# Optimization experiments

Measured on AMD Instinct MI355X. Metric: run time of the kernel, lower is better.

The kernel has to match this reference:

```python
import jax, jax.numpy as jnp
import numpy as np

NEG_SLOPE = 0.01  # torch nn.LeakyReLU default


def setup_inputs() -> dict:
    key = jax.random.key(0)
    k1, k2 = jax.random.split(key)
    B, L, N = 32, 512, 1024
    X = jax.random.normal(k1, (B, L, N), dtype=jnp.float32)
    W = jax.random.normal(k2, (1, 2 * L), dtype=jnp.float32) * (1.0 / np.sqrt(2 * L))
    return {"X": X, "W": W}


def reference(X, W):
    # X: [B, L, N]; W: [1, 2L] weight of Linear(2L, 1, bias=False)
    L = X.shape[1]
    N = X.shape[2]
    w1 = W[0, :L]   # applied to X[:, :, i]
    w2 = W[0, L:]   # applied to X[:, :, j]
    s1 = jnp.einsum('bln,l->bn', X, w1)  # [B, N]
    s2 = jnp.einsum('bln,l->bn', X, w2)  # [B, N]
    # e[b,i,j] = leaky_relu(s1[b,i] + s2[b,j]) for i != j, 0 on the diagonal
    e = jax.nn.leaky_relu(s1[:, :, None] + s2[:, None, :], NEG_SLOPE)  # [B, N, N]
    diag = jnp.eye(N, dtype=bool)
    e = jnp.where(diag[None, :, :], 0.0, e)
    # softmax over dim=1 (over i), matching torch.softmax(e, dim=1)
    alpha = jax.nn.softmax(e, axis=1)  # [B, N, N]
    # h = bmm(alpha, X^T)^T: h[b,l,i] = sum_j alpha[b,i,j] * X[b,l,j]
    h = jnp.einsum('bij,blj->bli', alpha, X)  # [B, L, N]
    return jax.nn.sigmoid(h)
```

## Files before the change

### kernel.cpp

```cpp
#include <hip/hip_runtime.h>
#include <hip/hip_bf16.h>

#define BATCH 32
#define LSEQ  512
#define NDIM  1024
#define NSPLIT 16

typedef __attribute__((ext_vector_type(8))) short bf16x8;
typedef __attribute__((ext_vector_type(4))) float f32x4;

__device__ __forceinline__ unsigned short f2bf(float x) {
    __hip_bfloat16 h = __float2bfloat16(x);
    return __builtin_bit_cast(unsigned short, h);
}

__global__ __launch_bounds__(256) void prep_kernel(
    const float* __restrict__ X, const float* __restrict__ W,
    unsigned short* __restrict__ Xb, float* __restrict__ P1, float* __restrict__ P2)
{
    __shared__ float sw[2 * LSEQ];
    int tid = threadIdx.x;
    for (int i = tid; i < 2 * LSEQ; i += 256) sw[i] = W[i];
    __syncthreads();

    int b  = blockIdx.y;
    int sp = blockIdx.x;
    int l0 = sp * (LSEQ / NSPLIT);
    size_t base = ((size_t)b * LSEQ + l0) * NDIM + tid * 4;
    const float* xp = X + base;
    unsigned short* xbp = Xb + base;

    float a0=0,a1=0,a2=0,a3=0, c0=0,c1=0,c2=0,c3=0;
    for (int l = 0; l < LSEQ / NSPLIT; ++l) {
        float4 x = *(const float4*)(xp + (size_t)l * NDIM);
        float w1 = sw[l0 + l], w2 = sw[LSEQ + l0 + l];
        a0 = fmaf(x.x, w1, a0); a1 = fmaf(x.y, w1, a1);
        a2 = fmaf(x.z, w1, a2); a3 = fmaf(x.w, w1, a3);
        c0 = fmaf(x.x, w2, c0); c1 = fmaf(x.y, w2, c1);
        c2 = fmaf(x.z, w2, c2); c3 = fmaf(x.w, w2, c3);
        ushort4 u; u.x = f2bf(x.x); u.y = f2bf(x.y); u.z = f2bf(x.z); u.w = f2bf(x.w);
        *(ushort4*)(xbp + (size_t)l * NDIM) = u;
    }
    size_t po = ((size_t)sp * BATCH + b) * NDIM + tid * 4;
    *(float4*)(P1 + po) = make_float4(a0, a1, a2, a3);
    *(float4*)(P2 + po) = make_float4(c0, c1, c2, c3);
}

__global__ __launch_bounds__(256) void stats_kernel(
    const float* __restrict__ P1, const float* __restrict__ P2,
    float* __restrict__ s1, float* __restrict__ s2, float* __restrict__ rd)
{
    __shared__ float s1s[NDIM];
    __shared__ float s2s[128];
    int t = threadIdx.x;
    int b = blockIdx.x >> 3, sl = blockIdx.x & 7;
    int j0 = sl * 128;

    #pragma unroll
    for (int q = 0; q < 4; ++q) {
        int n = q * 256 + t;
        float a = 0.f;
        #pragma unroll
        for (int sp = 0; sp < NSPLIT; ++sp)
            a += P1[((size_t)sp * BATCH + b) * NDIM + n];
        s1s[n] = a;
        if (sl == 0) s1[b * NDIM + n] = a;
    }
    if (t < 128) {
        int j = j0 + t;
        float c = 0.f;
        #pragma unroll
        for (int sp = 0; sp < NSPLIT; ++sp)
            c += P2[((size_t)sp * BATCH + b) * NDIM + j];
        s2s[t] = c;
        s2[b * NDIM + j] = c;
    }
    __syncthreads();

    int jl = t >> 1, half = t & 1;
    int jg = j0 + jl;
    float s2j = s2s[jl];
    float sum = 0.f;
    int i0 = half * 512;
    for (int i = i0; i < i0 + 512; ++i) {
        float v = s1s[i] + s2j;
        v = fmaxf(v, 0.01f * v);
        if (i == jg) v = 0.f;
        sum += __expf(v);
    }
    sum += __shfl_xor(sum, 1);
    if (half == 0) rd[b * NDIM + jg] = 1.0f / sum;
}

__global__ __launch_bounds__(256) void btgen_kernel(
    const float* __restrict__ s1, const float* __restrict__ s2,
    const float* __restrict__ rd, unsigned short* __restrict__ Bt)
{
    int wid = threadIdx.x >> 6, lane = threadIdx.x & 63;
    int r = blockIdx.x * 4 + wid;
    int b = r >> 10, i = r & 1023;
    float s1i = s1[r];
    const float* s2b = s2 + b * NDIM;
    const float* rdb = rd + b * NDIM;
    unsigned short* outp = Bt + (size_t)r * NDIM;

    #pragma unroll
    for (int q = 0; q < 2; ++q) {
        int j0 = q * 512 + lane * 8;
        float sv[8], rv[8];
        #pragma unroll
        for (int h = 0; h < 2; ++h) {
            float4 s4 = *(const float4*)(s2b + j0 + h * 4);
            float4 r4 = *(const float4*)(rdb + j0 + h * 4);
            sv[h*4+0]=s4.x; sv[h*4+1]=s4.y; sv[h*4+2]=s4.z; sv[h*4+3]=s4.w;
            rv[h*4+0]=r4.x; rv[h*4+1]=r4.y; rv[h*4+2]=r4.z; rv[h*4+3]=r4.w;
        }
        bf16x8 v;
        #pragma unroll
        for (int k = 0; k < 8; ++k) {
            float e = s1i + sv[k];
            e = fmaxf(e, 0.01f * e);
            if (j0 + k == i) e = 0.f;
            v[k] = (short)f2bf(__expf(e) * rv[k]);
        }
        *(bf16x8*)&outp[j0] = v;
    }
}

#define WAITVM(n) asm volatile("s_waitcnt vmcnt(" #n ")" ::: "memory")
#define FENCE()   asm volatile("" ::: "memory")

#define DO_STAGE(bufi) {                                                        \
    _Pragma("unroll")                                                           \
    for (int j = 0; j < 4; ++j) {                                               \
        __builtin_amdgcn_global_load_lds(                                       \
            (const __attribute__((address_space(1))) void*)srcp[j],             \
            (__attribute__((address_space(3))) void*)(LdsC + (bufi) * 32768 +   \
                                                      ldst0 + j * 8192),        \
            16, 0, 0);                                                          \
        srcp[j] += 64;                       \
    } }

#define COMPUTE(bufi) {                                                         \
    const char* Lb = LdsC + (bufi) * 32768;                                     \
    bf16x8 av[8]; bf16x8 bv[4];                                                 \
    _Pragma("unroll")                                                           \
    for (int mi = 0; mi < 8; ++mi)                                              \
        av[mi] = *(const bf16x8*)(Lb + abase0 + mi * 2048);                     \
    _Pragma("unroll")                                                           \
    for (int ni = 0; ni < 4; ++ni)                                              \
        bv[ni] = *(const bf16x8*)(Lb + bbase0 + ni * 2048);                     \
    __builtin_amdgcn_s_setprio(1);                                              \
    _Pragma("unroll")                                                           \
    for (int ni = 0; ni < 4; ++ni)                                              \
        _Pragma("unroll")                                                       \
        for (int mi = 0; mi < 8; ++mi)                                          \
            acc[mi][ni] = __builtin_amdgcn_mfma_f32_16x16x32_bf16(              \
                av[mi], bv[ni], acc[mi][ni], 0, 0, 0);                          \
    __builtin_amdgcn_s_setprio(0);                                              \
}

__global__ __launch_bounds__(512, 2) void gemm_kernel(
    const unsigned short* __restrict__ Xb, const unsigned short* __restrict__ Bt,
    float* __restrict__ out)
{
    __shared__ __align__(16) unsigned short LDSU[65536];
    char* LdsC = (char*)LDSU;

    const int tid = threadIdx.x, lane = tid & 63, wid = tid >> 6;
    const int wm = wid >> 2, wn = wid & 3;

    int flat  = blockIdx.x;
    int xcd   = flat & 7;
    int p     = flat >> 3;
    int b     = (p >> 3) * 8 + xcd;
    int inner = p & 7;
    int mt = inner & 1, nt = inner >> 1;
    int l0 = mt * 256, n0 = nt * 256;

    const char* XgB = (const char*)(Xb + ((size_t)b * LSEQ + l0) * NDIM);
    const char* BgB = (const char*)(Bt + ((size_t)b * NDIM + n0) * NDIM);

    const char* srcp[4];
    #pragma unroll
    for (int j = 0; j < 4; ++j) {
        int c = tid + j * 512;
        int r = c >> 3, slot = c & 7;
        int off = (slot * 16) ^ ((r & 7) << 4);
        srcp[j] = (off < 64) ? XgB + (size_t)r * 2048 + off
                             : BgB + (size_t)r * 2048 + (off - 64);
    }
    const int ldst0 = wid * 1024;

    const int rsel = lane & 15, kq = lane >> 4;
    const int swz  = (rsel & 7) << 4;
    const int abase0 = wm * 16384 + rsel * 128 + ((kq * 16) ^ swz);
    const int bbase0 = wn * 8192  + rsel * 128 + (((64 + kq * 16)) ^ swz);

    f32x4 acc[8][4] = {};

    DO_STAGE(0); DO_STAGE(1); DO_STAGE(2);

    for (int t = 0; t < 29; ++t) {
        WAITVM(8);
        __builtin_amdgcn_s_barrier();
        FENCE();
        DO_STAGE((t + 3) & 3);
        COMPUTE(t & 3);
    }
    WAITVM(8); __builtin_amdgcn_s_barrier(); FENCE(); COMPUTE(1);
    WAITVM(4); __builtin_amdgcn_s_barrier(); FENCE(); COMPUTE(2);
    WAITVM(0); __builtin_amdgcn_s_barrier(); FENCE(); COMPUTE(3);

    float* outb = out + ((size_t)b * LSEQ + l0) * NDIM + n0;
    const int rq = lane >> 4, cl = lane & 15;
    #pragma unroll
    for (int mi = 0; mi < 8; ++mi)
        #pragma unroll
        for (int ni = 0; ni < 4; ++ni) {
            int col = wn * 64 + ni * 16 + cl;
            #pragma unroll
            for (int r2 = 0; r2 < 4; ++r2) {
                int row = wm * 128 + mi * 16 + rq * 4 + r2;
                float v = acc[mi][ni][r2];
                outb[(size_t)row * NDIM + col] = 1.0f / (1.0f + __expf(-v));
            }
        }
}

#undef WAITVM
#undef FENCE
#undef DO_STAGE
#undef COMPUTE

extern "C" void kernel_launch(void* const* d_in, const int* in_sizes, int n_in,
                              void* d_out, int out_size, void* d_ws, size_t ws_size,
                              hipStream_t stream) {
    (void)in_sizes; (void)n_in; (void)out_size; (void)ws_size;
    const float* X = (const float*)d_in[0];
    const float* W = (const float*)d_in[1];
    float* out = (float*)d_out;

    float* s1 = (float*)d_ws;
    float* s2 = s1 + BATCH * NDIM;
    float* rd = s2 + BATCH * NDIM;
    float* P1 = rd + BATCH * NDIM;
    float* P2 = P1 + (size_t)NSPLIT * BATCH * NDIM;
    unsigned short* Xb = (unsigned short*)(P2 + (size_t)NSPLIT * BATCH * NDIM);
    unsigned short* Bt = Xb + (size_t)BATCH * LSEQ * NDIM;

    prep_kernel<<<dim3(NSPLIT, BATCH), 256, 0, stream>>>(X, W, Xb, P1, P2);
    stats_kernel<<<256, 256, 0, stream>>>(P1, P2, s1, s2, rd);
    btgen_kernel<<<(BATCH * NDIM) / 4, 256, 0, stream>>>(s1, s2, rd, Bt);
    gemm_kernel<<<256, 512, 0, stream>>>(Xb, Bt, out);
}
```

Before: 183.7 us.

## Split GEMM K-tile compute into two half phases with interleaved prefetch

Each K-step of the GEMM loop now runs as two halves of 4 M-subtiles each. Each half loads its A fragments, issues two of the four async global-to-LDS prefetch loads, and waits on LDS counters behind a sched barrier. A workgroup barrier sits between the halves. The aim is to spread the global load issue across the MFMA work and to lower the number of live A registers, in return for an extra barrier per iteration and explicit waitcnt/scheduling constraints.

```diff
diff --git a/kernel.cpp b/kernel.cpp
--- a/kernel.cpp
+++ b/kernel.cpp
@@ -128,35 +128,51 @@
 }
 
 #define WAITVM(n) asm volatile("s_waitcnt vmcnt(" #n ")" ::: "memory")
+#define LGKM0()   do { asm volatile("s_waitcnt lgkmcnt(0)" ::: "memory"); \
+                       __builtin_amdgcn_sched_barrier(0); } while (0)
 #define FENCE()   asm volatile("" ::: "memory")
 
-#define DO_STAGE(bufi) {                                                        \
-    _Pragma("unroll")                                                           \
-    for (int j = 0; j < 4; ++j) {                                               \
-        __builtin_amdgcn_global_load_lds(                                       \
-            (const __attribute__((address_space(1))) void*)srcp[j],             \
-            (__attribute__((address_space(3))) void*)(LdsC + (bufi) * 32768 +   \
-                                                      ldst0 + j * 8192),        \
-            16, 0, 0);                                                          \
-        srcp[j] += 64;                       \
-    } }
-
-#define COMPUTE(bufi) {                                                         \
+#define STAGE1(bufi, j_) {                                                      \
+    __builtin_amdgcn_global_load_lds(                                           \
+        (const __attribute__((address_space(1))) void*)srcp[j_],                \
+        (__attribute__((address_space(3))) void*)(LdsC + (bufi) * 32768 +       \
+                                                  ldst0 + (j_) * 8192),         \
+        16, 0, 0);                                                              \
+    srcp[j_] += 64;                                   \
+}
+
+#define TILE(bufi, pfbuf, PF) {                                                 \
     const char* Lb = LdsC + (bufi) * 32768;                                     \
-    bf16x8 av[8]; bf16x8 bv[4];                                                 \
-    _Pragma("unroll")                                                           \
-    for (int mi = 0; mi < 8; ++mi)                                              \
-        av[mi] = *(const bf16x8*)(Lb + abase0 + mi * 2048);                     \
+    bf16x8 av[4], bv[4];                                                        \
     _Pragma("unroll")                                                           \
     for (int ni = 0; ni < 4; ++ni)                                              \
         bv[ni] = *(const bf16x8*)(Lb + bbase0 + ni * 2048);                     \
+    _Pragma("unroll")                                                           \
+    for (int mi = 0; mi < 4; ++mi)                                              \
+        av[mi] = *(const bf16x8*)(Lb + abase0 + mi * 2048);                     \
+    if (PF) { STAGE1(pfbuf, 0); STAGE1(pfbuf, 1); }                             \
+    LGKM0();                                                                    \
     __builtin_amdgcn_s_setprio(1);                                              \
     _Pragma("unroll")                                                           \
     for (int ni = 0; ni < 4; ++ni)                                              \
         _Pragma("unroll")                                                       \
-        for (int mi = 0; mi < 8; ++mi)                                          \
+        for (int mi = 0; mi < 4; ++mi)                                          \
             acc[mi][ni] = __builtin_amdgcn_mfma_f32_16x16x32_bf16(              \
                 av[mi], bv[ni], acc[mi][ni], 0, 0, 0);                          \
+    __builtin_amdgcn_s_setprio(0);                                              \
+    FENCE(); __builtin_amdgcn_s_barrier(); FENCE();                             \
+    _Pragma("unroll")                                                           \
+    for (int mi = 0; mi < 4; ++mi)                                              \
+        av[mi] = *(const bf16x8*)(Lb + abase0 + (4 + mi) * 2048);               \
+    if (PF) { STAGE1(pfbuf, 2); STAGE1(pfbuf, 3); }                             \
+    LGKM0();                                                                    \
+    __builtin_amdgcn_s_setprio(1);                                              \
+    _Pragma("unroll")                                                           \
+    for (int ni = 0; ni < 4; ++ni)                                              \
+        _Pragma("unroll")                                                       \
+        for (int mi = 0; mi < 4; ++mi)                                          \
+            acc[4 + mi][ni] = __builtin_amdgcn_mfma_f32_16x16x32_bf16(          \
+                av[mi], bv[ni], acc[4 + mi][ni], 0, 0, 0);                      \
     __builtin_amdgcn_s_setprio(0);                                              \
 }
 
@@ -199,18 +215,18 @@
 
     f32x4 acc[8][4] = {};
 
-    DO_STAGE(0); DO_STAGE(1); DO_STAGE(2);
+    { STAGE1(0,0); STAGE1(0,1); STAGE1(0,2); STAGE1(0,3); }
+    { STAGE1(1,0); STAGE1(1,1); STAGE1(1,2); STAGE1(1,3); }
+    { STAGE1(2,0); STAGE1(2,1); STAGE1(2,2); STAGE1(2,3); }
 
     for (int t = 0; t < 29; ++t) {
         WAITVM(8);
-        __builtin_amdgcn_s_barrier();
-        FENCE();
-        DO_STAGE((t + 3) & 3);
-        COMPUTE(t & 3);
-    }
-    WAITVM(8); __builtin_amdgcn_s_barrier(); FENCE(); COMPUTE(1);
-    WAITVM(4); __builtin_amdgcn_s_barrier(); FENCE(); COMPUTE(2);
-    WAITVM(0); __builtin_amdgcn_s_barrier(); FENCE(); COMPUTE(3);
+        FENCE(); __builtin_amdgcn_s_barrier(); FENCE();
+        TILE(t & 3, (t + 3) & 3, 1);
+    }
+    WAITVM(8); FENCE(); __builtin_amdgcn_s_barrier(); FENCE(); TILE(1, 0, 0);
+    WAITVM(4); FENCE(); __builtin_amdgcn_s_barrier(); FENCE(); TILE(2, 0, 0);
+    WAITVM(0); FENCE(); __builtin_amdgcn_s_barrier(); FENCE(); TILE(3, 0, 0);
 
     float* outb = out + ((size_t)b * LSEQ + l0) * NDIM + n0;
     const int rq = lane >> 4, cl = lane & 15;
@@ -229,9 +245,10 @@
 }
 
 #undef WAITVM
+#undef LGKM0
 #undef FENCE
-#undef DO_STAGE
-#undef COMPUTE
+#undef STAGE1
+#undef TILE
 
 extern "C" void kernel_launch(void* const* d_in, const int* in_sizes, int n_in,
                               void* d_out, int out_size, void* d_ws, size_t ws_size,
```

New measurement: 185.9 us. About the same (+1.2%).

## Restructure GEMM to K=128 double-buffered tiles with interleaved staging; widen prep grid

Applied to the files above, without the earlier changes.

The GEMM main loop moves from a 4-stage ring of K=32 stages to two 64KB buffers holding K=128 tiles, each split into two K-halves. Global-to-LDS loads for upcoming tiles are interleaved between MFMA groups, with barriers and an lgkmcnt wait around each group, and the LDS swizzle is redone for 64-byte rows. Separately, prep_kernel gets a z dimension of 2 so each thread handles 2 columns instead of 4, doubling the block count to raise parallelism. The extra barriers per tile add synchronisation cost and the hand-written staging order must be correct to avoid races.

```diff
diff --git a/kernel.cpp b/kernel.cpp
--- a/kernel.cpp
+++ b/kernel.cpp
@@ -25,25 +25,26 @@
 
     int b  = blockIdx.y;
     int sp = blockIdx.x;
+    int z  = blockIdx.z;
     int l0 = sp * (LSEQ / NSPLIT);
-    size_t base = ((size_t)b * LSEQ + l0) * NDIM + tid * 4;
+    int n  = z * 512 + tid * 2;
+    size_t base = ((size_t)b * LSEQ + l0) * NDIM + n;
     const float* xp = X + base;
     unsigned short* xbp = Xb + base;
 
-    float a0=0,a1=0,a2=0,a3=0, c0=0,c1=0,c2=0,c3=0;
+    float a0 = 0, a1 = 0, c0 = 0, c1 = 0;
+    #pragma unroll 4
     for (int l = 0; l < LSEQ / NSPLIT; ++l) {
-        float4 x = *(const float4*)(xp + (size_t)l * NDIM);
+        float2 x = *(const float2*)(xp + (size_t)l * NDIM);
         float w1 = sw[l0 + l], w2 = sw[LSEQ + l0 + l];
         a0 = fmaf(x.x, w1, a0); a1 = fmaf(x.y, w1, a1);
-        a2 = fmaf(x.z, w1, a2); a3 = fmaf(x.w, w1, a3);
         c0 = fmaf(x.x, w2, c0); c1 = fmaf(x.y, w2, c1);
-        c2 = fmaf(x.z, w2, c2); c3 = fmaf(x.w, w2, c3);
-        ushort4 u; u.x = f2bf(x.x); u.y = f2bf(x.y); u.z = f2bf(x.z); u.w = f2bf(x.w);
-        *(ushort4*)(xbp + (size_t)l * NDIM) = u;
-    }
-    size_t po = ((size_t)sp * BATCH + b) * NDIM + tid * 4;
-    *(float4*)(P1 + po) = make_float4(a0, a1, a2, a3);
-    *(float4*)(P2 + po) = make_float4(c0, c1, c2, c3);
+        ushort2 u; u.x = f2bf(x.x); u.y = f2bf(x.y);
+        *(ushort2*)(xbp + (size_t)l * NDIM) = u;
+    }
+    size_t po = ((size_t)sp * BATCH + b) * NDIM + n;
+    *(float2*)(P1 + po) = make_float2(a0, a1);
+    *(float2*)(P2 + po) = make_float2(c0, c1);
 }
 
 __global__ __launch_bounds__(256) void stats_kernel(
@@ -128,36 +129,56 @@
 }
 
 #define WAITVM(n) asm volatile("s_waitcnt vmcnt(" #n ")" ::: "memory")
-#define FENCE()   asm volatile("" ::: "memory")
-
-#define DO_STAGE(bufi) {                                                        \
-    _Pragma("unroll")                                                           \
-    for (int j = 0; j < 4; ++j) {                                               \
-        __builtin_amdgcn_global_load_lds(                                       \
-            (const __attribute__((address_space(1))) void*)srcp[j],             \
-            (__attribute__((address_space(3))) void*)(LdsC + (bufi) * 32768 +   \
-                                                      ldst0 + j * 8192),        \
-            16, 0, 0);                                                          \
-        srcp[j] += 64;                       \
-    } }
-
-#define COMPUTE(bufi) {                                                         \
-    const char* Lb = LdsC + (bufi) * 32768;                                     \
-    bf16x8 av[8]; bf16x8 bv[4];                                                 \
-    _Pragma("unroll")                                                           \
-    for (int mi = 0; mi < 8; ++mi)                                              \
-        av[mi] = *(const bf16x8*)(Lb + abase0 + mi * 2048);                     \
-    _Pragma("unroll")                                                           \
-    for (int ni = 0; ni < 4; ++ni)                                              \
-        bv[ni] = *(const bf16x8*)(Lb + bbase0 + ni * 2048);                     \
-    __builtin_amdgcn_s_setprio(1);                                              \
-    _Pragma("unroll")                                                           \
-    for (int ni = 0; ni < 4; ++ni)                                              \
-        _Pragma("unroll")                                                       \
-        for (int mi = 0; mi < 8; ++mi)                                          \
-            acc[mi][ni] = __builtin_amdgcn_mfma_f32_16x16x32_bf16(              \
-                av[mi], bv[ni], acc[mi][ni], 0, 0, 0);                          \
-    __builtin_amdgcn_s_setprio(0);                                              \
+#define LGKM0()   asm volatile("s_waitcnt lgkmcnt(0)" ::: "memory")
+#define BARF()    do { asm volatile("" ::: "memory");                          \
+                       __builtin_amdgcn_s_barrier();                           \
+                       asm volatile("" ::: "memory"); } while (0)
+
+#define STAGE(PTR, OPB, KH, TT, DB) do {                                       \
+    const char* s_ = (PTR) + (TT) * 128 + (KH) * 64;                           \
+    __builtin_amdgcn_global_load_lds(                                          \
+        (const __attribute__((address_space(1))) void*)s_,                     \
+        (__attribute__((address_space(3))) void*)(LdsC + (DB) * 65536 + (OPB)  \
+            + (KH) * 16384 + tid * 16), 16, 0, 0);                             \
+    __builtin_amdgcn_global_load_lds(                                          \
+        (const __attribute__((address_space(1))) void*)(s_ + 262144),          \
+        (__attribute__((address_space(3))) void*)(LdsC + (DB) * 65536 + (OPB)  \
+            + (KH) * 16384 + 8192 + tid * 16), 16, 0, 0);                      \
+} while (0)
+
+#define RDA(DB, KH, MI) (*(const bf16x8*)(LdsC + (DB) * 65536 +                \
+                          (KH) * 16384 + abase + (MI) * 1024))
+#define RDB(DB, KH, NI) (*(const bf16x8*)(LdsC + (DB) * 65536 + 32768 +        \
+                          (KH) * 16384 + bbase + (NI) * 1024))
+
+#define MFMA16(NH)                                                             \
+    __builtin_amdgcn_s_setprio(1);                                             \
+    _Pragma("unroll")                                                          \
+    for (int ni2 = 0; ni2 < 2; ++ni2)                                          \
+        _Pragma("unroll")                                                      \
+        for (int mi = 0; mi < 8; ++mi)                                         \
+            acc[mi][(NH) * 2 + ni2] = __builtin_amdgcn_mfma_f32_16x16x32_bf16( \
+                av[mi], bv[ni2], acc[mi][(NH) * 2 + ni2], 0, 0, 0);            \
+    __builtin_amdgcn_s_setprio(0);
+
+#define TILE(TT, DB, SM) {                                                     \
+    bf16x8 av[8], bv[2];                                                       \
+    _Pragma("unroll")                                                          \
+    for (int mi = 0; mi < 8; ++mi) av[mi] = RDA(DB, 0, mi);                    \
+    bv[0] = RDB(DB, 0, 0); bv[1] = RDB(DB, 0, 1);                              \
+    if ((SM) >= 1) STAGE(pB, 32768, 1, (TT) + 1, (DB) ^ 1);                    \
+    BARF(); LGKM0(); MFMA16(0); BARF();                                        \
+    bv[0] = RDB(DB, 0, 2); bv[1] = RDB(DB, 0, 3);                              \
+    if ((SM) >= 2) STAGE(pA, 0, 0, (TT) + 2, DB);                              \
+    BARF(); LGKM0(); MFMA16(1); BARF();                                        \
+    _Pragma("unroll")                                                          \
+    for (int mi = 0; mi < 8; ++mi) av[mi] = RDA(DB, 1, mi);                    \
+    bv[0] = RDB(DB, 1, 0); bv[1] = RDB(DB, 1, 1);                              \
+    if ((SM) >= 2) STAGE(pB, 32768, 0, (TT) + 2, DB);                          \
+    BARF(); LGKM0(); MFMA16(0); BARF();                                        \
+    bv[0] = RDB(DB, 1, 2); bv[1] = RDB(DB, 1, 3);                              \
+    if ((SM) >= 2) STAGE(pA, 0, 1, (TT) + 2, DB);                              \
+    BARF(); LGKM0(); MFMA16(1);                                                \
 }
 
 __global__ __launch_bounds__(512, 2) void gemm_kernel(
@@ -167,7 +188,8 @@
     __shared__ __align__(16) unsigned short LDSU[65536];
     char* LdsC = (char*)LDSU;
 
-    const int tid = threadIdx.x, lane = tid & 63, wid = tid >> 6;
+    const int tid = threadIdx.x, lane = tid & 63;
+    const int wid = tid >> 6;
     const int wm = wid >> 2, wn = wid & 3;
 
     int flat  = blockIdx.x;
@@ -181,36 +203,36 @@
     const char* XgB = (const char*)(Xb + ((size_t)b * LSEQ + l0) * NDIM);
     const char* BgB = (const char*)(Bt + ((size_t)b * NDIM + n0) * NDIM);
 
-    const char* srcp[4];
-    #pragma unroll
-    for (int j = 0; j < 4; ++j) {
-        int c = tid + j * 512;
-        int r = c >> 3, slot = c & 7;
-        int off = (slot * 16) ^ ((r & 7) << 4);
-        srcp[j] = (off < 64) ? XgB + (size_t)r * 2048 + off
-                             : BgB + (size_t)r * 2048 + (off - 64);
-    }
-    const int ldst0 = wid * 1024;
+    {
+    }
+    const int srow  = tid >> 2;
+    const int sswz  = ((srow >> 1) & 3) << 4;
+    const int sloff = ((tid & 3) * 16) ^ sswz;
+    const char* pA = XgB + (size_t)srow * 2048 + sloff;
+    const char* pB = BgB + (size_t)srow * 2048 + sloff;
 
     const int rsel = lane & 15, kq = lane >> 4;
-    const int swz  = (rsel & 7) << 4;
-    const int abase0 = wm * 16384 + rsel * 128 + ((kq * 16) ^ swz);
-    const int bbase0 = wn * 8192  + rsel * 128 + (((64 + kq * 16)) ^ swz);
+    const int swz2 = ((rsel >> 1) & 3) << 4;
+    const int abase = (wm * 128 + rsel) * 64 + ((kq * 16) ^ swz2);
+    const int bbase = (wn * 64  + rsel) * 64 + ((kq * 16) ^ swz2);
 
     f32x4 acc[8][4] = {};
 
-    DO_STAGE(0); DO_STAGE(1); DO_STAGE(2);
-
-    for (int t = 0; t < 29; ++t) {
-        WAITVM(8);
-        __builtin_amdgcn_s_barrier();
-        FENCE();
-        DO_STAGE((t + 3) & 3);
-        COMPUTE(t & 3);
-    }
-    WAITVM(8); __builtin_amdgcn_s_barrier(); FENCE(); COMPUTE(1);
-    WAITVM(4); __builtin_amdgcn_s_barrier(); FENCE(); COMPUTE(2);
-    WAITVM(0); __builtin_amdgcn_s_barrier(); FENCE(); COMPUTE(3);
+    STAGE(pA, 0,     0, 0, 0);
+    STAGE(pB, 32768, 0, 0, 0);
+    STAGE(pA, 0,     1, 0, 0);
+    STAGE(pB, 32768, 1, 0, 0);
+    STAGE(pA, 0,     0, 1, 1);
+    STAGE(pB, 32768, 0, 1, 1);
+    STAGE(pA, 0,     1, 1, 1);
+
+    for (int pp = 0; pp < 7; ++pp) {
+        int t0 = 2 * pp;
+        WAITVM(6); BARF(); TILE(t0,     0, 2);
+        WAITVM(6); BARF(); TILE(t0 + 1, 1, 2);
+    }
+    WAITVM(6); BARF(); TILE(14, 0, 1);
+    WAITVM(0); BARF(); TILE(15, 1, 0);
 
     float* outb = out + ((size_t)b * LSEQ + l0) * NDIM + n0;
     const int rq = lane >> 4, cl = lane & 15;
@@ -229,9 +251,13 @@
 }
 
 #undef WAITVM
-#undef FENCE
-#undef DO_STAGE
-#undef COMPUTE
+#undef LGKM0
+#undef BARF
+#undef STAGE
+#undef RDA
+#undef RDB
+#undef MFMA16
+#undef TILE
 
 extern "C" void kernel_launch(void* const* d_in, const int* in_sizes, int n_in,
                               void* d_out, int out_size, void* d_ws, size_t ws_size,
@@ -249,7 +275,7 @@
     unsigned short* Xb = (unsigned short*)(P2 + (size_t)NSPLIT * BATCH * NDIM);
     unsigned short* Bt = Xb + (size_t)BATCH * LSEQ * NDIM;
 
-    prep_kernel<<<dim3(NSPLIT, BATCH), 256, 0, stream>>>(X, W, Xb, P1, P2);
+    prep_kernel<<<dim3(NSPLIT, BATCH, 2), 256, 0, stream>>>(X, W, Xb, P1, P2);
     stats_kernel<<<256, 256, 0, stream>>>(P1, P2, s1, s2, rd);
     btgen_kernel<<<(BATCH * NDIM) / 4, 256, 0, stream>>>(s1, s2, rd, Bt);
     gemm_kernel<<<256, 512, 0, stream>>>(Xb, Bt, out);
```

Result: no change. 186.2 us (+1.4%).

## Fuse attention-weight generation into GEMM, computing B tiles in LDS on the fly

Applied to the files above, without the earlier changes.

Drops the separate btgen kernel and the bf16 Bt matrix in global memory. The GEMM now builds each softmax-weight tile in LDS from s1, s2 and log-reciprocal denominators, while only X tiles are streamed from global memory. The normalisation is folded into the exponent as exp(v - log sum). The pipeline becomes double-buffered with 128-byte k-steps and interleaves B generation between the MFMA halves. Prep now uses NSPLIT 32 with an unrolled loop. This removes roughly a 64MB write and read of Bt, but adds exp work inside the GEMM, full waits each iteration, and much larger LDS use (136KB), which may limit occupancy below the declared 2 blocks.

```diff
diff --git a/kernel.cpp b/kernel.cpp
--- a/kernel.cpp
+++ b/kernel.cpp
@@ -4,7 +4,7 @@
 #define BATCH 32
 #define LSEQ  512
 #define NDIM  1024
-#define NSPLIT 16
+#define NSPLIT 32
 
 typedef __attribute__((ext_vector_type(8))) short bf16x8;
 typedef __attribute__((ext_vector_type(4))) float f32x4;
@@ -31,6 +31,7 @@
     unsigned short* xbp = Xb + base;
 
     float a0=0,a1=0,a2=0,a3=0, c0=0,c1=0,c2=0,c3=0;
+    #pragma unroll
     for (int l = 0; l < LSEQ / NSPLIT; ++l) {
         float4 x = *(const float4*)(xp + (size_t)l * NDIM);
         float w1 = sw[l0 + l], w2 = sw[LSEQ + l0 + l];
@@ -48,7 +49,7 @@
 
 __global__ __launch_bounds__(256) void stats_kernel(
     const float* __restrict__ P1, const float* __restrict__ P2,
-    float* __restrict__ s1, float* __restrict__ s2, float* __restrict__ rd)
+    float* __restrict__ s1, float* __restrict__ s2, float* __restrict__ lrd)
 {
     __shared__ float s1s[NDIM];
     __shared__ float s2s[128];
@@ -89,83 +90,79 @@
         sum += __expf(v);
     }
     sum += __shfl_xor(sum, 1);
-    if (half == 0) rd[b * NDIM + jg] = 1.0f / sum;
-}
-
-__global__ __launch_bounds__(256) void btgen_kernel(
-    const float* __restrict__ s1, const float* __restrict__ s2,
-    const float* __restrict__ rd, unsigned short* __restrict__ Bt)
-{
-    int wid = threadIdx.x >> 6, lane = threadIdx.x & 63;
-    int r = blockIdx.x * 4 + wid;
-    int b = r >> 10, i = r & 1023;
-    float s1i = s1[r];
-    const float* s2b = s2 + b * NDIM;
-    const float* rdb = rd + b * NDIM;
-    unsigned short* outp = Bt + (size_t)r * NDIM;
-
-    #pragma unroll
-    for (int q = 0; q < 2; ++q) {
-        int j0 = q * 512 + lane * 8;
-        float sv[8], rv[8];
-        #pragma unroll
-        for (int h = 0; h < 2; ++h) {
-            float4 s4 = *(const float4*)(s2b + j0 + h * 4);
-            float4 r4 = *(const float4*)(rdb + j0 + h * 4);
-            sv[h*4+0]=s4.x; sv[h*4+1]=s4.y; sv[h*4+2]=s4.z; sv[h*4+3]=s4.w;
-            rv[h*4+0]=r4.x; rv[h*4+1]=r4.y; rv[h*4+2]=r4.z; rv[h*4+3]=r4.w;
-        }
-        bf16x8 v;
-        #pragma unroll
-        for (int k = 0; k < 8; ++k) {
-            float e = s1i + sv[k];
-            e = fmaxf(e, 0.01f * e);
-            if (j0 + k == i) e = 0.f;
-            v[k] = (short)f2bf(__expf(e) * rv[k]);
-        }
-        *(bf16x8*)&outp[j0] = v;
-    }
-}
-
-#define WAITVM(n) asm volatile("s_waitcnt vmcnt(" #n ")" ::: "memory")
-#define FENCE()   asm volatile("" ::: "memory")
-
-#define DO_STAGE(bufi) {                                                        \
-    _Pragma("unroll")                                                           \
-    for (int j = 0; j < 4; ++j) {                                               \
-        __builtin_amdgcn_global_load_lds(                                       \
-            (const __attribute__((address_space(1))) void*)srcp[j],             \
-            (__attribute__((address_space(3))) void*)(LdsC + (bufi) * 32768 +   \
-                                                      ldst0 + j * 8192),        \
-            16, 0, 0);                                                          \
-        srcp[j] += 64;                       \
+    if (half == 0) lrd[b * NDIM + jg] = -__logf(sum);
+}
+
+#define WAITVM0() asm volatile("s_waitcnt vmcnt(0)" ::: "memory")
+#define LGKM0()   asm volatile("s_waitcnt lgkmcnt(0)" ::: "memory")
+#define BARF()    do { asm volatile("" ::: "memory");                          \
+                       __builtin_amdgcn_s_barrier();                           \
+                       asm volatile("" ::: "memory"); } while (0)
+
+#define STAGE(DB) {                                                            \
+    _Pragma("unroll")                                                          \
+    for (int j = 0; j < 4; ++j) {                                              \
+        __builtin_amdgcn_global_load_lds(                                      \
+            (const __attribute__((address_space(1))) void*)srcp[j],            \
+            (__attribute__((address_space(3))) void*)(LdsC + (DB) * 32768 +    \
+                tid * 16 + j * 8192), 16, 0, 0);                               \
+        srcp[j] += 128;                                  \
     } }
 
-#define COMPUTE(bufi) {                                                         \
-    const char* Lb = LdsC + (bufi) * 32768;                                     \
-    bf16x8 av[8]; bf16x8 bv[4];                                                 \
-    _Pragma("unroll")                                                           \
-    for (int mi = 0; mi < 8; ++mi)                                              \
-        av[mi] = *(const bf16x8*)(Lb + abase0 + mi * 2048);                     \
-    _Pragma("unroll")                                                           \
-    for (int ni = 0; ni < 4; ++ni)                                              \
-        bv[ni] = *(const bf16x8*)(Lb + bbase0 + ni * 2048);                     \
-    __builtin_amdgcn_s_setprio(1);                                              \
-    _Pragma("unroll")                                                           \
-    for (int ni = 0; ni < 4; ++ni)                                              \
-        _Pragma("unroll")                                                       \
-        for (int mi = 0; mi < 8; ++mi)                                          \
-            acc[mi][ni] = __builtin_amdgcn_mfma_f32_16x16x32_bf16(              \
-                av[mi], bv[ni], acc[mi][ni], 0, 0, 0);                          \
-    __builtin_amdgcn_s_setprio(0);                                              \
+#define BGEN(T2, DB) {                                                         \
+    const float* s2p = s2s + (T2) * 64 + jb * 8;                               \
+    const float* ldp = lrds + (T2) * 64 + jb * 8;                              \
+    float4 sa = *(const float4*)(s2p);                                         \
+    float4 sb = *(const float4*)(s2p + 4);                                     \
+    float4 la = *(const float4*)(ldp);                                         \
+    float4 lb = *(const float4*)(ldp + 4);                                     \
+    float sv[8] = {sa.x,sa.y,sa.z,sa.w,sb.x,sb.y,sb.z,sb.w};                   \
+    float lv[8] = {la.x,la.y,la.z,la.w,lb.x,lb.y,lb.z,lb.w};                   \
+    int jg0 = (T2) * 64 + jb * 8;                                              \
+    _Pragma("unroll")                                                          \
+    for (int q = 0; q < 4; ++q) {                                              \
+        int rloc = wid * 32 + q * 8 + il;                                      \
+        int ig = n0 + rloc;                                                    \
+        bf16x8 w;                                                              \
+        _Pragma("unroll")                                                      \
+        for (int h = 0; h < 8; ++h) {                                          \
+            float v = s1q[q] + sv[h];                                          \
+            v = fmaxf(v, 0.01f * v);                           \
+            if (jg0 + h == ig) v = 0.f;                  \
+            w[h] = (short)f2bf(__expf(v + lv[h]));                             \
+        }                                                                      \
+        *(bf16x8*)(LdsC + 65536 + (DB) * 32768 + rloc * 128 +                  \
+                   ((jb * 16) ^ (il << 4))) = w;                               \
+    } }
+
+#define COMPUTE_KS(DB, KOF) {                                                  \
+    bf16x8 av[8], bv[4];                                                       \
+    _Pragma("unroll")                                                          \
+    for (int mi = 0; mi < 8; ++mi)                                             \
+        av[mi] = *(const bf16x8*)(LdsC + (DB) * 32768 + arow + mi * 2048 +     \
+                                  (KOF));                                      \
+    _Pragma("unroll")                                                          \
+    for (int ni = 0; ni < 4; ++ni)                                             \
+        bv[ni] = *(const bf16x8*)(LdsC + 65536 + (DB) * 32768 + brow +         \
+                                  ni * 2048 + (KOF));                          \
+    __builtin_amdgcn_s_setprio(1);                                             \
+    _Pragma("unroll")                                                          \
+    for (int ni = 0; ni < 4; ++ni)                                             \
+        _Pragma("unroll")                                                      \
+        for (int mi = 0; mi < 8; ++mi)                                         \
+            acc[mi][ni] = __builtin_amdgcn_mfma_f32_16x16x32_bf16(             \
+                av[mi], bv[ni], acc[mi][ni], 0, 0, 0);                         \
+    __builtin_amdgcn_s_setprio(0);                                             \
 }
 
 __global__ __launch_bounds__(512, 2) void gemm_kernel(
-    const unsigned short* __restrict__ Xb, const unsigned short* __restrict__ Bt,
+    const unsigned short* __restrict__ Xb, const float* __restrict__ s1,
+    const float* __restrict__ s2, const float* __restrict__ lrd,
     float* __restrict__ out)
 {
-    __shared__ __align__(16) unsigned short LDSU[65536];
-    char* LdsC = (char*)LDSU;
+    __shared__ __align__(16) char LdsC[139264];
+    float* s2s  = (float*)(LdsC + 131072);
+    float* lrds = (float*)(LdsC + 135168);
 
     const int tid = threadIdx.x, lane = tid & 63, wid = tid >> 6;
     const int wm = wid >> 2, wn = wid & 3;
@@ -179,38 +176,53 @@
     int l0 = mt * 256, n0 = nt * 256;
 
     const char* XgB = (const char*)(Xb + ((size_t)b * LSEQ + l0) * NDIM);
-    const char* BgB = (const char*)(Bt + ((size_t)b * NDIM + n0) * NDIM);
 
     const char* srcp[4];
     #pragma unroll
     for (int j = 0; j < 4; ++j) {
         int c = tid + j * 512;
         int r = c >> 3, slot = c & 7;
-        int off = (slot * 16) ^ ((r & 7) << 4);
-        srcp[j] = (off < 64) ? XgB + (size_t)r * 2048 + off
-                             : BgB + (size_t)r * 2048 + (off - 64);
-    }
-    const int ldst0 = wid * 1024;
+        srcp[j] = XgB + (size_t)r * 2048 + ((slot * 16) ^ ((r & 7) << 4));
+    }
 
     const int rsel = lane & 15, kq = lane >> 4;
     const int swz  = (rsel & 7) << 4;
-    const int abase0 = wm * 16384 + rsel * 128 + ((kq * 16) ^ swz);
-    const int bbase0 = wn * 8192  + rsel * 128 + (((64 + kq * 16)) ^ swz);
+    const int kof0 = (kq * 16) ^ swz;
+    const int kof1 = (64 + kq * 16) ^ swz;
+    const int arow = (wm * 128 + rsel) * 128;
+    const int brow = (wn * 64 + rsel) * 128;
+
+    const int jb = lane & 7, il = lane >> 3;
+
+    {
+        const float* s2g = s2 + (size_t)b * NDIM;
+        const float* ldg = lrd + (size_t)b * NDIM;
+        if (tid < 256) *(float4*)(s2s + tid * 4) = *(const float4*)(s2g + tid * 4);
+        else *(float4*)(lrds + (tid - 256) * 4) = *(const float4*)(ldg + (tid - 256) * 4);
+    }
+    STAGE(0);
+    __syncthreads();
+
+    float s1q[4];
+    #pragma unroll
+    for (int q = 0; q < 4; ++q)
+        s1q[q] = s1[(size_t)b * NDIM + n0 + wid * 32 + q * 8 + il];
 
     f32x4 acc[8][4] = {};
 
-    DO_STAGE(0); DO_STAGE(1); DO_STAGE(2);
-
-    for (int t = 0; t < 29; ++t) {
-        WAITVM(8);
-        __builtin_amdgcn_s_barrier();
-        FENCE();
-        DO_STAGE((t + 3) & 3);
-        COMPUTE(t & 3);
-    }
-    WAITVM(8); __builtin_amdgcn_s_barrier(); FENCE(); COMPUTE(1);
-    WAITVM(4); __builtin_amdgcn_s_barrier(); FENCE(); COMPUTE(2);
-    WAITVM(0); __builtin_amdgcn_s_barrier(); FENCE(); COMPUTE(3);
+    BGEN(0, 0);
+    LGKM0(); BARF();
+
+    for (int t = 0; t < 15; ++t) {
+        int db = t & 1, dn = db ^ 1;
+        STAGE(dn);
+        COMPUTE_KS(db, kof0);
+        BGEN(t + 1, dn);
+        COMPUTE_KS(db, kof1);
+        LGKM0(); WAITVM0(); BARF();
+    }
+    COMPUTE_KS(1, kof0);
+    COMPUTE_KS(1, kof1);
 
     float* outb = out + ((size_t)b * LSEQ + l0) * NDIM + n0;
     const int rq = lane >> 4, cl = lane & 15;
@@ -228,10 +240,12 @@
         }
 }
 
-#undef WAITVM
-#undef FENCE
-#undef DO_STAGE
-#undef COMPUTE
+#undef WAITVM0
+#undef LGKM0
+#undef BARF
+#undef STAGE
+#undef BGEN
+#undef COMPUTE_KS
 
 extern "C" void kernel_launch(void* const* d_in, const int* in_sizes, int n_in,
                               void* d_out, int out_size, void* d_ws, size_t ws_size,
@@ -243,14 +257,12 @@
 
     float* s1 = (float*)d_ws;
     float* s2 = s1 + BATCH * NDIM;
-    float* rd = s2 + BATCH * NDIM;
-    float* P1 = rd + BATCH * NDIM;
+    float* lrd = s2 + BATCH * NDIM;
+    float* P1 = lrd + BATCH * NDIM;
     float* P2 = P1 + (size_t)NSPLIT * BATCH * NDIM;
     unsigned short* Xb = (unsigned short*)(P2 + (size_t)NSPLIT * BATCH * NDIM);
-    unsigned short* Bt = Xb + (size_t)BATCH * LSEQ * NDIM;
 
     prep_kernel<<<dim3(NSPLIT, BATCH), 256, 0, stream>>>(X, W, Xb, P1, P2);
-    stats_kernel<<<256, 256, 0, stream>>>(P1, P2, s1, s2, rd);
-    btgen_kernel<<<(BATCH * NDIM) / 4, 256, 0, stream>>>(s1, s2, rd, Bt);
-    gemm_kernel<<<256, 512, 0, stream>>>(Xb, Bt, out);
-}
+    stats_kernel<<<256, 256, 0, stream>>>(P1, P2, s1, s2, lrd);
+    gemm_kernel<<<256, 512, 0, stream>>>(Xb, s1, s2, lrd, out);
+}
```

Result: slower. 189.1 us (+2.9%).
